# Kernel tuning notes

Hardware: AMD Instinct MI355X
Metric: run time of the kernel (lower is better)

## Reference

```python
import jax, jax.numpy as jnp
import numpy as np

B, S, D, H, FF = 2, 2048, 1024, 16, 4096
HD = D // H
SCALE = 1.0 / np.sqrt(HD).astype(np.float32)
EPS = 1e-5


def _ln(x, g, b):
    m = jnp.mean(x, axis=-1, keepdims=True)
    v = jnp.mean((x - m) ** 2, axis=-1, keepdims=True)
    return (x - m) * jax.lax.rsqrt(v + EPS) * g + b


def setup_inputs() -> dict:
    key = jax.random.key(0)
    ks = jax.random.split(key, 8)
    def lin(k, fan_in, shape):
        return (jax.random.normal(k, shape, jnp.float32) / np.sqrt(fan_in)).astype(jnp.float32)
    return {
        "x": jax.random.normal(ks[0], (B, S, D), jnp.float32),
        "w_qkv": lin(ks[1], D, (D, 3 * D)),          # qkv_proj (no bias)
        "w_o": lin(ks[2], D, (D, D)),                 # out_proj
        "b_o": jnp.zeros((D,), jnp.float32),
        "g1": jnp.ones((D,), jnp.float32),            # attn LayerNorm
        "bt1": jnp.zeros((D,), jnp.float32),
        "w1": lin(ks[3], D, (D, FF)),                 # FFN linear1
        "b1": jnp.zeros((FF,), jnp.float32),
        "w2": lin(ks[4], FF, (FF, D)),                # FFN linear2
        "b2": jnp.zeros((D,), jnp.float32),
        "g2": jnp.ones((D,), jnp.float32),            # FFN LayerNorm
        "bt2": jnp.zeros((D,), jnp.float32),
    }


def reference(x, w_qkv, w_o, b_o, g1, bt1, w1, b1, w2, b2, g2, bt2):
    # --- MultiHeadAttention (post-LN, dropout=eval/identity) ---
    qkv = (x @ w_qkv).reshape(B, S, H, 3 * HD)
    q, k, v = jnp.split(qkv, 3, axis=-1)  # each [B,S,H,HD]
    # kernel_func = scaled softmax over keys
    scores = jnp.einsum("bihd,bjhd->bhij", q, k) * SCALE  # [B,H,S,S]
    attn = jax.nn.softmax(scores, axis=-1)
    ao = jnp.einsum("bhij,bjhd->bihd", attn, v).reshape(B, S, D)
    y = _ln(x + ao @ w_o + b_o, g1, bt1)
    # --- FFN (post-LN) ---
    h = jax.nn.relu(y @ w1 + b1)
    return _ln(y + h @ w2 + b2, g2, bt2)
```

## Files before the change

kernel.cpp:

```cpp
#include <hip/hip_runtime.h>
#include <hip/hip_bf16.h>

#define B_  2
#define S_  2048
#define D_  1024
#define H_  16
#define HD_ 64
#define FF_ 4096
#define NT  (B_ * S_)
#define SCALE_ 0.125f
#define KLOG2E 0.1803368801111f
#define EPS_  1e-5f

typedef __attribute__((ext_vector_type(8))) short bf16x8;
typedef __attribute__((ext_vector_type(4))) float f32x4;

__device__ inline short f2bf(float f) {
    __hip_bfloat16 h = __float2bfloat16(f);
    return __builtin_bit_cast(short, h);
}
__device__ inline float bf2f(unsigned short u) {
    __hip_bfloat16 h = __builtin_bit_cast(__hip_bfloat16, u);
    return __bfloat162float(h);
}

#define GLOBAL_AS __attribute__((address_space(1)))
#define LDS_AS    __attribute__((address_space(3)))

struct DetectArgs { const unsigned short* p[12]; int n[12]; };

__global__ __launch_bounds__(256) void detect_kernel(DetectArgs a, int* flags) {
    const int t = blockIdx.x;
    const unsigned short* s = a.p[t];
    const int cnt = min(a.n[t], 16384);
    const int tid = threadIdx.x;
    int huge = 0, zeven = 0;
    for (int i = tid; i < cnt; i += 256) {
        const unsigned short v = s[i];
        const int e = (v >> 7) & 0xFF;
        if (e >= 142) huge++;
        if (((i & 1) == 0) && ((v & 0x7FFF) == 0)) zeven++;
    }
    __shared__ int sh, sz;
    if (tid == 0) { sh = 0; sz = 0; }
    __syncthreads();
    atomicAdd(&sh, huge);
    atomicAdd(&sz, zeven);
    __syncthreads();
    if (tid == 0) flags[t] = (sh > 0 || sz * 4 > cnt) ? 1 : 0;
}

__global__ __launch_bounds__(256) void conv_bf16_kernel(
    const void* __restrict__ src, unsigned short* __restrict__ dst, int n,
    const int* __restrict__ flags, int fidx)
{
    const int i = blockIdx.x * 256 + threadIdx.x;
    if (i >= n) return;
    if (flags[fidx])
        dst[i] = (unsigned short)f2bf(((const float*)src)[i]);
    else
        dst[i] = ((const unsigned short*)src)[i];
}

__global__ __launch_bounds__(256) void conv_t_kernel(
    const void* __restrict__ src, unsigned short* __restrict__ dst,
    int K, int N, const int* __restrict__ flags, int fidx)
{
    __shared__ short T[32][33];
    const int kt = blockIdx.x * 32, nt = blockIdx.y * 32;
    const int c  = threadIdx.x & 31;
    const int r0 = (threadIdx.x >> 5) * 4;
    const int f  = flags[fidx];
#pragma unroll
    for (int i = 0; i < 4; i++) {
        const int r = r0 + i;
        const size_t gi = (size_t)(kt + r) * N + nt + c;
        short v = f ? f2bf(((const float*)src)[gi])
                    : (short)((const unsigned short*)src)[gi];
        T[c][r] = v;
    }
    __syncthreads();
#pragma unroll
    for (int i = 0; i < 4; i++) {
        const int n = r0 + i;
        dst[(size_t)(nt + n) * K + kt + c] = (unsigned short)T[n][c];
    }
}

struct VecArgs { const void* src[7]; float* dst[7]; int n[7]; int fidx[7]; };

__global__ __launch_bounds__(256) void conv_vecs_kernel(VecArgs a,
                                                        const int* __restrict__ flags) {
#pragma unroll
    for (int v = 0; v < 7; v++) {
        const int f = flags[a.fidx[v]];
        for (int i = blockIdx.x * 256 + threadIdx.x; i < a.n[v]; i += gridDim.x * 256) {
            a.dst[v][i] = f ? ((const float*)a.src[v])[i]
                            : bf2f(((const unsigned short*)a.src[v])[i]);
        }
    }
}

template<bool HAS_BIAS, bool RELU, int RES, bool OUT_F32, bool QSCALE>
__global__ __launch_bounds__(256) void gemm128_kernel(
    const unsigned short* __restrict__ A,
    const unsigned short* __restrict__ Bt,
    const float* __restrict__ bias,
    const unsigned short* __restrict__ resb,
    const float* __restrict__ resf,
    const int* __restrict__ flags,
    void* __restrict__ out,
    int M, int N, int K)
{
    __shared__ short As[128 * 32];
    __shared__ short Bs[128 * 32];

    const int tid  = threadIdx.x;
    const int wave = tid >> 6;
    const int lane = tid & 63;
    const int quad = lane >> 4;
    const int l16  = lane & 15;

    const int row0 = blockIdx.x * 128;
    const int col0 = blockIdx.y * 128;

    const int ldrow = lane >> 2;
    const int ldk   = (lane & 3) * 8;
    const unsigned short* agp0 = A  + (size_t)(row0 + wave * 32 + ldrow) * K + ldk;
    const unsigned short* agp1 = agp0 + (size_t)16 * K;
    const unsigned short* bgp0 = Bt + (size_t)(col0 + wave * 32 + ldrow) * K + ldk;
    const unsigned short* bgp1 = bgp0 + (size_t)16 * K;
    LDS_AS void* alds0 = (LDS_AS void*)&As[wave * 1024 + lane * 8];
    LDS_AS void* alds1 = (LDS_AS void*)&As[wave * 1024 + 512 + lane * 8];
    LDS_AS void* blds0 = (LDS_AS void*)&Bs[wave * 1024 + lane * 8];
    LDS_AS void* blds1 = (LDS_AS void*)&Bs[wave * 1024 + 512 + lane * 8];

    const int wm = (wave >> 1) * 64;
    const int wn = (wave & 1) * 64;

    f32x4 acc[4][4] = {};

    for (int k0 = 0; k0 < K; k0 += 32) {
        __builtin_amdgcn_global_load_lds(
            (const GLOBAL_AS void*)(agp0 + k0), alds0, 16, 0, 0);
        __builtin_amdgcn_global_load_lds(
            (const GLOBAL_AS void*)(agp1 + k0), alds1, 16, 0, 0);
        __builtin_amdgcn_global_load_lds(
            (const GLOBAL_AS void*)(bgp0 + k0), blds0, 16, 0, 0);
        __builtin_amdgcn_global_load_lds(
            (const GLOBAL_AS void*)(bgp1 + k0), blds1, 16, 0, 0);
        __syncthreads();

        bf16x8 af[4], bfr[4];
#pragma unroll
        for (int mi = 0; mi < 4; mi++)
            af[mi] = *reinterpret_cast<const bf16x8*>(
                &As[(wm + mi * 16 + l16) * 32 + quad * 8]);
#pragma unroll
        for (int ni = 0; ni < 4; ni++)
            bfr[ni] = *reinterpret_cast<const bf16x8*>(
                &Bs[(wn + ni * 16 + l16) * 32 + quad * 8]);
#pragma unroll
        for (int mi = 0; mi < 4; mi++)
#pragma unroll
            for (int ni = 0; ni < 4; ni++)
                acc[mi][ni] = __builtin_amdgcn_mfma_f32_16x16x32_bf16(
                    af[mi], bfr[ni], acc[mi][ni], 0, 0, 0);
        __syncthreads();
    }

    int resIsF32 = 0;
    if constexpr (RES == 2) resIsF32 = flags[0];

#pragma unroll
    for (int ni = 0; ni < 4; ni++) {
        const int col = col0 + wn + ni * 16 + l16;
        float badd = 0.f;
        if constexpr (HAS_BIAS) badd = bias[col];
        float qs = 1.f;
        if constexpr (QSCALE)
            qs = (((col0 + wn + ni * 16) % 192) < 64) ? KLOG2E : 1.f;
#pragma unroll
        for (int mi = 0; mi < 4; mi++) {
#pragma unroll
            for (int r = 0; r < 4; r++) {
                const int row = row0 + wm + mi * 16 + quad * 4 + r;
                float v = acc[mi][ni][r] + badd;
                if constexpr (QSCALE) v *= qs;
                if constexpr (RES == 1) {
                    v += bf2f(resb[(size_t)row * N + col]);
                } else if constexpr (RES == 2) {
                    v += resIsF32 ? resf[(size_t)row * N + col]
                                  : bf2f(resb[(size_t)row * N + col]);
                }
                if constexpr (RELU) v = fmaxf(v, 0.f);
                if constexpr (OUT_F32)
                    ((float*)out)[(size_t)row * N + col] = v;
                else
                    ((unsigned short*)out)[(size_t)row * N + col] =
                        (unsigned short)f2bf(v);
            }
        }
    }
}

__global__ __launch_bounds__(256) void gemm128_sk_kernel(
    const unsigned short* __restrict__ A,
    const unsigned short* __restrict__ Bt,
    float* __restrict__ out0,
    float* __restrict__ out1,
    int M, int N, int K)
{
    __shared__ short As[128 * 32];
    __shared__ short Bs[128 * 32];

    const int tid  = threadIdx.x;
    const int wave = tid >> 6;
    const int lane = tid & 63;
    const int quad = lane >> 4;
    const int l16  = lane & 15;

    const int row0 = blockIdx.x * 128;
    const int col0 = blockIdx.y * 128;
    const int z    = blockIdx.z;
    const int Kh   = K >> 1;

    const unsigned short* Az  = A  + (size_t)z * Kh;
    const unsigned short* Btz = Bt + (size_t)z * Kh;
    float* out = z ? out1 : out0;

    const int ldrow = lane >> 2;
    const int ldk   = (lane & 3) * 8;
    const unsigned short* agp0 = Az  + (size_t)(row0 + wave * 32 + ldrow) * K + ldk;
    const unsigned short* agp1 = agp0 + (size_t)16 * K;
    const unsigned short* bgp0 = Btz + (size_t)(col0 + wave * 32 + ldrow) * K + ldk;
    const unsigned short* bgp1 = bgp0 + (size_t)16 * K;
    LDS_AS void* alds0 = (LDS_AS void*)&As[wave * 1024 + lane * 8];
    LDS_AS void* alds1 = (LDS_AS void*)&As[wave * 1024 + 512 + lane * 8];
    LDS_AS void* blds0 = (LDS_AS void*)&Bs[wave * 1024 + lane * 8];
    LDS_AS void* blds1 = (LDS_AS void*)&Bs[wave * 1024 + 512 + lane * 8];

    const int wm = (wave >> 1) * 64;
    const int wn = (wave & 1) * 64;

    f32x4 acc[4][4] = {};

    for (int k0 = 0; k0 < Kh; k0 += 32) {
        __builtin_amdgcn_global_load_lds(
            (const GLOBAL_AS void*)(agp0 + k0), alds0, 16, 0, 0);
        __builtin_amdgcn_global_load_lds(
            (const GLOBAL_AS void*)(agp1 + k0), alds1, 16, 0, 0);
        __builtin_amdgcn_global_load_lds(
            (const GLOBAL_AS void*)(bgp0 + k0), blds0, 16, 0, 0);
        __builtin_amdgcn_global_load_lds(
            (const GLOBAL_AS void*)(bgp1 + k0), blds1, 16, 0, 0);
        __syncthreads();

        bf16x8 af[4], bfr[4];
#pragma unroll
        for (int mi = 0; mi < 4; mi++)
            af[mi] = *reinterpret_cast<const bf16x8*>(
                &As[(wm + mi * 16 + l16) * 32 + quad * 8]);
#pragma unroll
        for (int ni = 0; ni < 4; ni++)
            bfr[ni] = *reinterpret_cast<const bf16x8*>(
                &Bs[(wn + ni * 16 + l16) * 32 + quad * 8]);
#pragma unroll
        for (int mi = 0; mi < 4; mi++)
#pragma unroll
            for (int ni = 0; ni < 4; ni++)
                acc[mi][ni] = __builtin_amdgcn_mfma_f32_16x16x32_bf16(
                    af[mi], bfr[ni], acc[mi][ni], 0, 0, 0);
        __syncthreads();
    }

#pragma unroll
    for (int ni = 0; ni < 4; ni++) {
        const int col = col0 + wn + ni * 16 + l16;
#pragma unroll
        for (int mi = 0; mi < 4; mi++)
#pragma unroll
            for (int r = 0; r < 4; r++) {
                const int row = row0 + wm + mi * 16 + quad * 4 + r;
                out[(size_t)row * N + col] = acc[mi][ni][r];
            }
    }
}

__global__ __launch_bounds__(256) void attn_kernel(
    const unsigned short* __restrict__ qkv,
    unsigned short* __restrict__ ao)
{
    const int qt = blockIdx.x;
    const int h  = blockIdx.y;
    const int b  = blockIdx.z;

    const int tid  = threadIdx.x;
    const int wave = tid >> 6;
    const int lane = tid & 63;
    const int quad = lane >> 4;
    const int l16  = lane & 15;

    __shared__ short Ks[64 * 72];
    __shared__ short Vt[64 * 72];
    __shared__ short Ps[4 * 32 * 72];

    bf16x8 qf[2][2];
#pragma unroll
    for (int mi = 0; mi < 2; mi++) {
        const int qrow = qt * 128 + wave * 32 + mi * 16 + l16;
        const unsigned short* qb = qkv + (size_t)(b * S_ + qrow) * 3072 + h * 192;
        qf[mi][0] = *reinterpret_cast<const bf16x8*>(qb + quad * 8);
        qf[mi][1] = *reinterpret_cast<const bf16x8*>(qb + 32 + quad * 8);
    }

    f32x4 o[2][4] = {};
    float l_[2][4] = {};

    const int skey = tid >> 3;
    const int soct = tid & 7;
    const int vp   = tid >> 3;
    const int kA   = (vp & 15) + ((vp >> 4) << 5);
    const int kB   = kA + 16;
    const int posA = 4 * (vp & 15) + 2 * (vp >> 4);
    const int vwr  = ((posA >> 3) ^ soct) * 8 + (posA & 7);

    const int pb = wave * (32 * 72);

    const unsigned short* kbase0 = qkv + (size_t)(b * S_) * 3072 + h * 192 + 64;
    const unsigned short* vbase0 = qkv + (size_t)(b * S_) * 3072 + h * 192 + 128;

    bf16x8 pk0 = *reinterpret_cast<const bf16x8*>(kbase0 + (size_t)skey * 3072 + soct * 8);
    bf16x8 pk1 = *reinterpret_cast<const bf16x8*>(kbase0 + (size_t)(skey + 32) * 3072 + soct * 8);
    bf16x8 pv0 = *reinterpret_cast<const bf16x8*>(vbase0 + (size_t)kA * 3072 + soct * 8);
    bf16x8 pv1 = *reinterpret_cast<const bf16x8*>(vbase0 + (size_t)kB * 3072 + soct * 8);

    for (int kb = 0; kb < S_; kb += 64) {
        {
            const int woct0 = soct ^ ((skey >> 3) & 1);
            *reinterpret_cast<bf16x8*>(&Ks[skey * 72 + woct0 * 8]) = pk0;
            const int woct1 = soct ^ (((skey + 32) >> 3) & 1);
            *reinterpret_cast<bf16x8*>(&Ks[(skey + 32) * 72 + woct1 * 8]) = pk1;
#pragma unroll
            for (int j = 0; j < 8; j++) {
                const int d = soct * 8 + j;
                const unsigned int val =
                    (unsigned int)(unsigned short)pv0[j] |
                    ((unsigned int)(unsigned short)pv1[j] << 16);
                *reinterpret_cast<unsigned int*>(&Vt[d * 72 + vwr]) = val;
            }
        }
        __syncthreads();

        {
            const int kbn = (kb + 64 < S_) ? kb + 64 : kb;
            pk0 = *reinterpret_cast<const bf16x8*>(
                kbase0 + (size_t)(kbn + skey) * 3072 + soct * 8);
            pk1 = *reinterpret_cast<const bf16x8*>(
                kbase0 + (size_t)(kbn + skey + 32) * 3072 + soct * 8);
            pv0 = *reinterpret_cast<const bf16x8*>(
                vbase0 + (size_t)(kbn + kA) * 3072 + soct * 8);
            pv1 = *reinterpret_cast<const bf16x8*>(
                vbase0 + (size_t)(kbn + kB) * 3072 + soct * 8);
        }

        f32x4 s[2][4] = {};
#pragma unroll
        for (int c2 = 0; c2 < 2; c2++) {
#pragma unroll
            for (int nt = 0; nt < 4; nt++) {
                const int key = nt * 16 + l16;
                const int roct = (c2 * 4 + quad) ^ ((key >> 3) & 1);
                bf16x8 kf = *reinterpret_cast<const bf16x8*>(
                    &Ks[key * 72 + roct * 8]);
                s[0][nt] = __builtin_amdgcn_mfma_f32_16x16x32_bf16(qf[0][c2], kf, s[0][nt], 0, 0, 0);
                s[1][nt] = __builtin_amdgcn_mfma_f32_16x16x32_bf16(qf[1][c2], kf, s[1][nt], 0, 0, 0);
            }
        }

#pragma unroll
        for (int mi = 0; mi < 2; mi++) {
#pragma unroll
            for (int r = 0; r < 4; r++) {
                const int m = mi * 16 + quad * 4 + r;
                float p0 = exp2f(s[mi][0][r]);
                float p1 = exp2f(s[mi][1][r]);
                float p2 = exp2f(s[mi][2][r]);
                float p3 = exp2f(s[mi][3][r]);
                l_[mi][r] += (p0 + p1) + (p2 + p3);
                uint2 w;
                w.x = (unsigned int)(unsigned short)f2bf(p0) |
                      ((unsigned int)(unsigned short)f2bf(p1) << 16);
                w.y = (unsigned int)(unsigned short)f2bf(p2) |
                      ((unsigned int)(unsigned short)f2bf(p3) << 16);
                *reinterpret_cast<uint2*>(&Ps[pb + m * 72 + l16 * 4]) = w;
            }
        }

#pragma unroll
        for (int c2 = 0; c2 < 2; c2++) {
            bf16x8 pf[2];
#pragma unroll
            for (int mi = 0; mi < 2; mi++) {
                const int m = mi * 16 + l16;
                pf[mi] = *reinterpret_cast<const bf16x8*>(
                    &Ps[pb + m * 72 + c2 * 32 + quad * 8]);
            }
#pragma unroll
            for (int ct = 0; ct < 4; ct++) {
                const int row = ct * 16 + l16;
                const int blk = (c2 * 4 + quad) ^ (row >> 3);
                bf16x8 vf = *reinterpret_cast<const bf16x8*>(
                    &Vt[row * 72 + blk * 8]);
                o[0][ct] = __builtin_amdgcn_mfma_f32_16x16x32_bf16(pf[0], vf, o[0][ct], 0, 0, 0);
                o[1][ct] = __builtin_amdgcn_mfma_f32_16x16x32_bf16(pf[1], vf, o[1][ct], 0, 0, 0);
            }
        }
        __syncthreads();
    }

    float rl[2][4];
#pragma unroll
    for (int mi = 0; mi < 2; mi++)
#pragma unroll
        for (int r = 0; r < 4; r++) {
            float l = l_[mi][r];
            l += __shfl_xor(l, 1);
            l += __shfl_xor(l, 2);
            l += __shfl_xor(l, 4);
            l += __shfl_xor(l, 8);
            rl[mi][r] = 1.f / l;
        }

#pragma unroll
    for (int mi = 0; mi < 2; mi++)
#pragma unroll
        for (int ct = 0; ct < 4; ct++)
#pragma unroll
            for (int r = 0; r < 4; r++) {
                const int row = qt * 128 + wave * 32 + mi * 16 + quad * 4 + r;
                ao[(size_t)(b * S_ + row) * D_ + h * HD_ + ct * 16 + l16] =
                    (unsigned short)f2bf(o[mi][ct][r] * rl[mi][r]);
            }
}

template<int RESM, bool FLAG_OUT>
__global__ __launch_bounds__(256) void ln_sum_kernel(
    const float* __restrict__ p0,
    const float* __restrict__ p1,
    const float* __restrict__ bias,
    const unsigned short* __restrict__ resb,
    const float* __restrict__ resf,
    const float* __restrict__ g,
    const float* __restrict__ bt,
    const int* __restrict__ flags,
    void* __restrict__ out)
{
    const int row = blockIdx.x;
    const int tid = threadIdx.x;
    const int c0  = tid * 4;
    const size_t base = (size_t)row * D_ + c0;

    float4 a = *reinterpret_cast<const float4*>(p0 + base);
    float4 bq = *reinterpret_cast<const float4*>(p1 + base);
    float4 bi = *reinterpret_cast<const float4*>(bias + c0);

    float v[4] = {a.x + bq.x + bi.x, a.y + bq.y + bi.y,
                  a.z + bq.z + bi.z, a.w + bq.w + bi.w};

    if constexpr (RESM == 1) {
        if (flags[0]) {
            float4 rv = *reinterpret_cast<const float4*>(resf + base);
            v[0] += rv.x; v[1] += rv.y; v[2] += rv.z; v[3] += rv.w;
        } else {
            uint2 rv = *reinterpret_cast<const uint2*>(resb + base);
            v[0] += bf2f((unsigned short)(rv.x & 0xFFFF));
            v[1] += bf2f((unsigned short)(rv.x >> 16));
            v[2] += bf2f((unsigned short)(rv.y & 0xFFFF));
            v[3] += bf2f((unsigned short)(rv.y >> 16));
        }
    } else {
        uint2 rv = *reinterpret_cast<const uint2*>(resb + base);
        v[0] += bf2f((unsigned short)(rv.x & 0xFFFF));
        v[1] += bf2f((unsigned short)(rv.x >> 16));
        v[2] += bf2f((unsigned short)(rv.y & 0xFFFF));
        v[3] += bf2f((unsigned short)(rv.y >> 16));
    }

    float s = v[0] + v[1] + v[2] + v[3];
    float sq = v[0] * v[0] + v[1] * v[1] + v[2] * v[2] + v[3] * v[3];
#pragma unroll
    for (int msk = 1; msk < 64; msk <<= 1) {
        s += __shfl_xor(s, msk);
        sq += __shfl_xor(sq, msk);
    }
    __shared__ float ss[4], ssq[4];
    if ((tid & 63) == 0) { ss[tid >> 6] = s; ssq[tid >> 6] = sq; }
    __syncthreads();
    s = ss[0] + ss[1] + ss[2] + ss[3];
    sq = ssq[0] + ssq[1] + ssq[2] + ssq[3];

    const float mean = s * (1.f / D_);
    const float var = sq * (1.f / D_) - mean * mean;
    const float rinv = rsqrtf(var + EPS_);

    int outF32 = 0;
    if constexpr (FLAG_OUT) outF32 = flags[0];

#pragma unroll
    for (int i = 0; i < 4; i++) {
        const int c = c0 + i;
        const float val = (v[i] - mean) * rinv * g[c] + bt[c];
        if constexpr (FLAG_OUT) {
            if (outF32) ((float*)out)[(size_t)row * D_ + c] = val;
            else ((unsigned short*)out)[(size_t)row * D_ + c] = (unsigned short)f2bf(val);
        } else {
            ((unsigned short*)out)[(size_t)row * D_ + c] = (unsigned short)f2bf(val);
        }
    }
}

extern "C" void kernel_launch(void* const* d_in, const int* in_sizes, int n_in,
                              void* d_out, int out_size, void* d_ws, size_t ws_size,
                              hipStream_t stream) {
    char* ws = (char*)d_ws;

    int*            flags = (int*)(ws + 0);
    unsigned short* xb    = (unsigned short*)(ws + 256);
    unsigned short* wqkvT = (unsigned short*)(ws + 8388864);
    unsigned short* woT   = (unsigned short*)(ws + 14680320);
    unsigned short* w1T   = (unsigned short*)(ws + 16777472);
    unsigned short* w2T   = (unsigned short*)(ws + 25166080);
    float*          bof   = (float*)(ws + 33554688);
    float*          g1f   = (float*)(ws + 33558784);
    float*          bt1f  = (float*)(ws + 33562880);
    float*          b1f   = (float*)(ws + 33566976);
    float*          b2f   = (float*)(ws + 33583360);
    float*          g2f   = (float*)(ws + 33587456);
    float*          bt2f  = (float*)(ws + 33591552);
    unsigned short* qkv   = (unsigned short*)(ws + 33595648);
    unsigned short* ao    = (unsigned short*)(ws + 256);
    unsigned short* y     = (unsigned short*)(ws + 33595648);
    unsigned short* hbuf  = (unsigned short*)(ws + 41984256);
    float*          part0 = (float*)(ws + 58761472);
    float*          part1 = (float*)(ws + 75538688);
    float*          hpart0= (float*)(ws + 256);

    dim3 blk(256);

    DetectArgs da;
    for (int i = 0; i < 12; i++) {
        da.p[i] = (const unsigned short*)d_in[i];
        da.n[i] = in_sizes[i];
    }
    detect_kernel<<<dim3(12), blk, 0, stream>>>(da, flags);

    conv_bf16_kernel<<<dim3((NT * D_ + 255) / 256), blk, 0, stream>>>(
        d_in[0], xb, NT * D_, flags, 0);
    conv_t_kernel<<<dim3(D_ / 32, 3 * D_ / 32), blk, 0, stream>>>(
        d_in[1], wqkvT, D_, 3 * D_, flags, 1);
    conv_t_kernel<<<dim3(D_ / 32, D_ / 32), blk, 0, stream>>>(
        d_in[2], woT, D_, D_, flags, 2);
    conv_t_kernel<<<dim3(D_ / 32, FF_ / 32), blk, 0, stream>>>(
        d_in[6], w1T, D_, FF_, flags, 6);
    conv_t_kernel<<<dim3(FF_ / 32, D_ / 32), blk, 0, stream>>>(
        d_in[8], w2T, FF_, D_, flags, 8);
    VecArgs va;
    const int vidx[7] = {3, 4, 5, 7, 9, 10, 11};
    float* vdst[7] = {bof, g1f, bt1f, b1f, b2f, g2f, bt2f};
    for (int i = 0; i < 7; i++) {
        va.src[i] = d_in[vidx[i]];
        va.dst[i] = vdst[i];
        va.n[i]   = in_sizes[vidx[i]];
        va.fidx[i] = vidx[i];
    }
    conv_vecs_kernel<<<dim3(16), blk, 0, stream>>>(va, flags);

    gemm128_kernel<false, false, 0, false, true>
        <<<dim3(NT / 128, 3072 / 128), blk, 0, stream>>>(
            xb, wqkvT, nullptr, nullptr, nullptr, flags, qkv, NT, 3072, 1024);

    attn_kernel<<<dim3(S_ / 128, H_, B_), blk, 0, stream>>>(qkv, ao);

    gemm128_sk_kernel<<<dim3(NT / 128, 1024 / 128, 2), blk, 0, stream>>>(
        ao, woT, part0, part1, NT, 1024, 1024);

    ln_sum_kernel<1, false><<<dim3(NT), blk, 0, stream>>>(
        part0, part1, bof, (const unsigned short*)d_in[0], (const float*)d_in[0],
        g1f, bt1f, flags, y);

    gemm128_kernel<true, true, 0, false, false>
        <<<dim3(NT / 128, 4096 / 128), blk, 0, stream>>>(
            y, w1T, b1f, nullptr, nullptr, flags, hbuf, NT, 4096, 1024);

    gemm128_sk_kernel<<<dim3(NT / 128, 1024 / 128, 2), blk, 0, stream>>>(
        hbuf, w2T, hpart0, part1, NT, 1024, 4096);

    ln_sum_kernel<2, true><<<dim3(NT), blk, 0, stream>>>(
        hpart0, part1, b2f, y, nullptr, g2f, bt2f, flags, d_out);
}
```

Baseline: 439.8 us.

## Merge conversion launches, deepen GEMM K-step, compute softmax denominators via MFMA

Several unrelated changes. The conversion launches are merged: the x conversion absorbs the vector conversions, and the four weight transposes become one launch. Both GEMM kernels now load two 32-wide K slices per barrier pair, which halves the number of syncs at the cost of doubled LDS. The attention kernel gets its row sums from an extra MFMA against a vector of ones instead of scalar adds and shuffles, and it packs bf16 pairs with a paired conversion. The LayerNorm store is vectorised.

```diff
diff --git a/kernel.cpp b/kernel.cpp
--- a/kernel.cpp
+++ b/kernel.cpp
@@ -22,6 +22,12 @@
 __device__ inline float bf2f(unsigned short u) {
     __hip_bfloat16 h = __builtin_bit_cast(__hip_bfloat16, u);
     return __bfloat162float(h);
+}
+__device__ inline unsigned int pk2bf(float lo, float hi) {
+    __hip_bfloat162 h = __float22bfloat162_rn(float2{lo, hi});
+    const unsigned short l16 = __builtin_bit_cast(unsigned short, h.x);
+    const unsigned short h16 = __builtin_bit_cast(unsigned short, h.y);
+    return (unsigned int)l16 | ((unsigned int)h16 << 16);
 }
 
 #define GLOBAL_AS __attribute__((address_space(1)))
@@ -50,27 +56,53 @@
     if (tid == 0) flags[t] = (sh > 0 || sz * 4 > cnt) ? 1 : 0;
 }
 
-__global__ __launch_bounds__(256) void conv_bf16_kernel(
+struct VecArgs { const void* src[7]; float* dst[7]; int n[7]; int fidx[7]; };
+
+__global__ __launch_bounds__(256) void conv_x_vecs_kernel(
     const void* __restrict__ src, unsigned short* __restrict__ dst, int n,
-    const int* __restrict__ flags, int fidx)
+    VecArgs a, const int* __restrict__ flags)
 {
     const int i = blockIdx.x * 256 + threadIdx.x;
-    if (i >= n) return;
-    if (flags[fidx])
-        dst[i] = (unsigned short)f2bf(((const float*)src)[i]);
-    else
-        dst[i] = ((const unsigned short*)src)[i];
-}
-
-__global__ __launch_bounds__(256) void conv_t_kernel(
-    const void* __restrict__ src, unsigned short* __restrict__ dst,
-    int K, int N, const int* __restrict__ flags, int fidx)
+    if (i < n) {
+        if (flags[0])
+            dst[i] = (unsigned short)f2bf(((const float*)src)[i]);
+        else
+            dst[i] = ((const unsigned short*)src)[i];
+    }
+    if (blockIdx.x < 7) {
+        const int v = blockIdx.x;
+        const int f = flags[a.fidx[v]];
+        for (int j = threadIdx.x; j < a.n[v]; j += 256) {
+            a.dst[v][j] = f ? ((const float*)a.src[v])[j]
+                            : bf2f(((const unsigned short*)a.src[v])[j]);
+        }
+    }
+}
+
+struct TArgs {
+    const void* src[4]; unsigned short* dst[4];
+    int K[4], N[4], fidx[4], start[5];
+};
+
+__global__ __launch_bounds__(256) void conv_t_all_kernel(
+    TArgs t, const int* __restrict__ flags)
 {
     __shared__ short T[32][33];
-    const int kt = blockIdx.x * 32, nt = blockIdx.y * 32;
+    const int tile = blockIdx.x;
+    int w = 0;
+    if (tile >= t.start[1]) w = 1;
+    if (tile >= t.start[2]) w = 2;
+    if (tile >= t.start[3]) w = 3;
+    const int rel = tile - t.start[w];
+    const int K = t.K[w], N = t.N[w];
+    const int tilesN = N / 32;
+    const int kt = (rel / tilesN) * 32, nt = (rel % tilesN) * 32;
+    const void* src = t.src[w];
+    unsigned short* dst = t.dst[w];
+    const int f = flags[t.fidx[w]];
+
     const int c  = threadIdx.x & 31;
     const int r0 = (threadIdx.x >> 5) * 4;
-    const int f  = flags[fidx];
 #pragma unroll
     for (int i = 0; i < 4; i++) {
         const int r = r0 + i;
@@ -84,20 +116,6 @@
     for (int i = 0; i < 4; i++) {
         const int n = r0 + i;
         dst[(size_t)(nt + n) * K + kt + c] = (unsigned short)T[n][c];
-    }
-}
-
-struct VecArgs { const void* src[7]; float* dst[7]; int n[7]; int fidx[7]; };
-
-__global__ __launch_bounds__(256) void conv_vecs_kernel(VecArgs a,
-                                                        const int* __restrict__ flags) {
-#pragma unroll
-    for (int v = 0; v < 7; v++) {
-        const int f = flags[a.fidx[v]];
-        for (int i = blockIdx.x * 256 + threadIdx.x; i < a.n[v]; i += gridDim.x * 256) {
-            a.dst[v][i] = f ? ((const float*)a.src[v])[i]
-                            : bf2f(((const unsigned short*)a.src[v])[i]);
-        }
     }
 }
 
@@ -112,8 +130,8 @@
     void* __restrict__ out,
     int M, int N, int K)
 {
-    __shared__ short As[128 * 32];
-    __shared__ short Bs[128 * 32];
+    __shared__ short As[2][128 * 32];
+    __shared__ short Bs[2][128 * 32];
 
     const int tid  = threadIdx.x;
     const int wave = tid >> 6;
@@ -130,42 +148,48 @@
     const unsigned short* agp1 = agp0 + (size_t)16 * K;
     const unsigned short* bgp0 = Bt + (size_t)(col0 + wave * 32 + ldrow) * K + ldk;
     const unsigned short* bgp1 = bgp0 + (size_t)16 * K;
-    LDS_AS void* alds0 = (LDS_AS void*)&As[wave * 1024 + lane * 8];
-    LDS_AS void* alds1 = (LDS_AS void*)&As[wave * 1024 + 512 + lane * 8];
-    LDS_AS void* blds0 = (LDS_AS void*)&Bs[wave * 1024 + lane * 8];
-    LDS_AS void* blds1 = (LDS_AS void*)&Bs[wave * 1024 + 512 + lane * 8];
 
     const int wm = (wave >> 1) * 64;
     const int wn = (wave & 1) * 64;
 
     f32x4 acc[4][4] = {};
 
-    for (int k0 = 0; k0 < K; k0 += 32) {
-        __builtin_amdgcn_global_load_lds(
-            (const GLOBAL_AS void*)(agp0 + k0), alds0, 16, 0, 0);
-        __builtin_amdgcn_global_load_lds(
-            (const GLOBAL_AS void*)(agp1 + k0), alds1, 16, 0, 0);
-        __builtin_amdgcn_global_load_lds(
-            (const GLOBAL_AS void*)(bgp0 + k0), blds0, 16, 0, 0);
-        __builtin_amdgcn_global_load_lds(
-            (const GLOBAL_AS void*)(bgp1 + k0), blds1, 16, 0, 0);
+    for (int k0 = 0; k0 < K; k0 += 64) {
+#pragma unroll
+        for (int h = 0; h < 2; h++) {
+            __builtin_amdgcn_global_load_lds(
+                (const GLOBAL_AS void*)(agp0 + k0 + h * 32),
+                (LDS_AS void*)&As[h][wave * 1024 + lane * 8], 16, 0, 0);
+            __builtin_amdgcn_global_load_lds(
+                (const GLOBAL_AS void*)(agp1 + k0 + h * 32),
+                (LDS_AS void*)&As[h][wave * 1024 + 512 + lane * 8], 16, 0, 0);
+            __builtin_amdgcn_global_load_lds(
+                (const GLOBAL_AS void*)(bgp0 + k0 + h * 32),
+                (LDS_AS void*)&Bs[h][wave * 1024 + lane * 8], 16, 0, 0);
+            __builtin_amdgcn_global_load_lds(
+                (const GLOBAL_AS void*)(bgp1 + k0 + h * 32),
+                (LDS_AS void*)&Bs[h][wave * 1024 + 512 + lane * 8], 16, 0, 0);
+        }
         __syncthreads();
 
-        bf16x8 af[4], bfr[4];
-#pragma unroll
-        for (int mi = 0; mi < 4; mi++)
-            af[mi] = *reinterpret_cast<const bf16x8*>(
-                &As[(wm + mi * 16 + l16) * 32 + quad * 8]);
-#pragma unroll
-        for (int ni = 0; ni < 4; ni++)
-            bfr[ni] = *reinterpret_cast<const bf16x8*>(
-                &Bs[(wn + ni * 16 + l16) * 32 + quad * 8]);
-#pragma unroll
-        for (int mi = 0; mi < 4; mi++)
+#pragma unroll
+        for (int h = 0; h < 2; h++) {
+            bf16x8 af[4], bfr[4];
+#pragma unroll
+            for (int mi = 0; mi < 4; mi++)
+                af[mi] = *reinterpret_cast<const bf16x8*>(
+                    &As[h][(wm + mi * 16 + l16) * 32 + quad * 8]);
 #pragma unroll
             for (int ni = 0; ni < 4; ni++)
-                acc[mi][ni] = __builtin_amdgcn_mfma_f32_16x16x32_bf16(
-                    af[mi], bfr[ni], acc[mi][ni], 0, 0, 0);
+                bfr[ni] = *reinterpret_cast<const bf16x8*>(
+                    &Bs[h][(wn + ni * 16 + l16) * 32 + quad * 8]);
+#pragma unroll
+            for (int mi = 0; mi < 4; mi++)
+#pragma unroll
+                for (int ni = 0; ni < 4; ni++)
+                    acc[mi][ni] = __builtin_amdgcn_mfma_f32_16x16x32_bf16(
+                        af[mi], bfr[ni], acc[mi][ni], 0, 0, 0);
+        }
         __syncthreads();
     }
 
@@ -211,8 +235,8 @@
     float* __restrict__ out1,
     int M, int N, int K)
 {
-    __shared__ short As[128 * 32];
-    __shared__ short Bs[128 * 32];
+    __shared__ short As[2][128 * 32];
+    __shared__ short Bs[2][128 * 32];
 
     const int tid  = threadIdx.x;
     const int wave = tid >> 6;
@@ -235,42 +259,48 @@
     const unsigned short* agp1 = agp0 + (size_t)16 * K;
     const unsigned short* bgp0 = Btz + (size_t)(col0 + wave * 32 + ldrow) * K + ldk;
     const unsigned short* bgp1 = bgp0 + (size_t)16 * K;
-    LDS_AS void* alds0 = (LDS_AS void*)&As[wave * 1024 + lane * 8];
-    LDS_AS void* alds1 = (LDS_AS void*)&As[wave * 1024 + 512 + lane * 8];
-    LDS_AS void* blds0 = (LDS_AS void*)&Bs[wave * 1024 + lane * 8];
-    LDS_AS void* blds1 = (LDS_AS void*)&Bs[wave * 1024 + 512 + lane * 8];
 
     const int wm = (wave >> 1) * 64;
     const int wn = (wave & 1) * 64;
 
     f32x4 acc[4][4] = {};
 
-    for (int k0 = 0; k0 < Kh; k0 += 32) {
-        __builtin_amdgcn_global_load_lds(
-            (const GLOBAL_AS void*)(agp0 + k0), alds0, 16, 0, 0);
-        __builtin_amdgcn_global_load_lds(
-            (const GLOBAL_AS void*)(agp1 + k0), alds1, 16, 0, 0);
-        __builtin_amdgcn_global_load_lds(
-            (const GLOBAL_AS void*)(bgp0 + k0), blds0, 16, 0, 0);
-        __builtin_amdgcn_global_load_lds(
-            (const GLOBAL_AS void*)(bgp1 + k0), blds1, 16, 0, 0);
+    for (int k0 = 0; k0 < Kh; k0 += 64) {
+#pragma unroll
+        for (int h = 0; h < 2; h++) {
+            __builtin_amdgcn_global_load_lds(
+                (const GLOBAL_AS void*)(agp0 + k0 + h * 32),
+                (LDS_AS void*)&As[h][wave * 1024 + lane * 8], 16, 0, 0);
+            __builtin_amdgcn_global_load_lds(
+                (const GLOBAL_AS void*)(agp1 + k0 + h * 32),
+                (LDS_AS void*)&As[h][wave * 1024 + 512 + lane * 8], 16, 0, 0);
+            __builtin_amdgcn_global_load_lds(
+                (const GLOBAL_AS void*)(bgp0 + k0 + h * 32),
+                (LDS_AS void*)&Bs[h][wave * 1024 + lane * 8], 16, 0, 0);
+            __builtin_amdgcn_global_load_lds(
+                (const GLOBAL_AS void*)(bgp1 + k0 + h * 32),
+                (LDS_AS void*)&Bs[h][wave * 1024 + 512 + lane * 8], 16, 0, 0);
+        }
         __syncthreads();
 
-        bf16x8 af[4], bfr[4];
-#pragma unroll
-        for (int mi = 0; mi < 4; mi++)
-            af[mi] = *reinterpret_cast<const bf16x8*>(
-                &As[(wm + mi * 16 + l16) * 32 + quad * 8]);
-#pragma unroll
-        for (int ni = 0; ni < 4; ni++)
-            bfr[ni] = *reinterpret_cast<const bf16x8*>(
-                &Bs[(wn + ni * 16 + l16) * 32 + quad * 8]);
-#pragma unroll
-        for (int mi = 0; mi < 4; mi++)
+#pragma unroll
+        for (int h = 0; h < 2; h++) {
+            bf16x8 af[4], bfr[4];
+#pragma unroll
+            for (int mi = 0; mi < 4; mi++)
+                af[mi] = *reinterpret_cast<const bf16x8*>(
+                    &As[h][(wm + mi * 16 + l16) * 32 + quad * 8]);
 #pragma unroll
             for (int ni = 0; ni < 4; ni++)
-                acc[mi][ni] = __builtin_amdgcn_mfma_f32_16x16x32_bf16(
-                    af[mi], bfr[ni], acc[mi][ni], 0, 0, 0);
+                bfr[ni] = *reinterpret_cast<const bf16x8*>(
+                    &Bs[h][(wn + ni * 16 + l16) * 32 + quad * 8]);
+#pragma unroll
+            for (int mi = 0; mi < 4; mi++)
+#pragma unroll
+                for (int ni = 0; ni < 4; ni++)
+                    acc[mi][ni] = __builtin_amdgcn_mfma_f32_16x16x32_bf16(
+                        af[mi], bfr[ni], acc[mi][ni], 0, 0, 0);
+        }
         __syncthreads();
     }
 
@@ -314,8 +344,12 @@
         qf[mi][1] = *reinterpret_cast<const bf16x8*>(qb + 32 + quad * 8);
     }
 
+    bf16x8 vones;
+#pragma unroll
+    for (int j = 0; j < 8; j++) vones[j] = (short)0x3F80;
+
     f32x4 o[2][4] = {};
-    float l_[2][4] = {};
+    f32x4 o_l[2] = {};
 
     const int skey = tid >> 3;
     const int soct = tid & 7;
@@ -383,16 +417,13 @@
 #pragma unroll
             for (int r = 0; r < 4; r++) {
                 const int m = mi * 16 + quad * 4 + r;
-                float p0 = exp2f(s[mi][0][r]);
-                float p1 = exp2f(s[mi][1][r]);
-                float p2 = exp2f(s[mi][2][r]);
-                float p3 = exp2f(s[mi][3][r]);
-                l_[mi][r] += (p0 + p1) + (p2 + p3);
+                const float p0 = exp2f(s[mi][0][r]);
+                const float p1 = exp2f(s[mi][1][r]);
+                const float p2 = exp2f(s[mi][2][r]);
+                const float p3 = exp2f(s[mi][3][r]);
                 uint2 w;
-                w.x = (unsigned int)(unsigned short)f2bf(p0) |
-                      ((unsigned int)(unsigned short)f2bf(p1) << 16);
-                w.y = (unsigned int)(unsigned short)f2bf(p2) |
-                      ((unsigned int)(unsigned short)f2bf(p3) << 16);
+                w.x = pk2bf(p0, p1);
+                w.y = pk2bf(p2, p3);
                 *reinterpret_cast<uint2*>(&Ps[pb + m * 72 + l16 * 4]) = w;
             }
         }
@@ -415,33 +446,26 @@
                 o[0][ct] = __builtin_amdgcn_mfma_f32_16x16x32_bf16(pf[0], vf, o[0][ct], 0, 0, 0);
                 o[1][ct] = __builtin_amdgcn_mfma_f32_16x16x32_bf16(pf[1], vf, o[1][ct], 0, 0, 0);
             }
+            o_l[0] = __builtin_amdgcn_mfma_f32_16x16x32_bf16(pf[0], vones, o_l[0], 0, 0, 0);
+            o_l[1] = __builtin_amdgcn_mfma_f32_16x16x32_bf16(pf[1], vones, o_l[1], 0, 0, 0);
         }
         __syncthreads();
     }
 
-    float rl[2][4];
-#pragma unroll
-    for (int mi = 0; mi < 2; mi++)
-#pragma unroll
-        for (int r = 0; r < 4; r++) {
-            float l = l_[mi][r];
-            l += __shfl_xor(l, 1);
-            l += __shfl_xor(l, 2);
-            l += __shfl_xor(l, 4);
-            l += __shfl_xor(l, 8);
-            rl[mi][r] = 1.f / l;
-        }
-
-#pragma unroll
-    for (int mi = 0; mi < 2; mi++)
+#pragma unroll
+    for (int mi = 0; mi < 2; mi++) {
+        f32x4 rl;
+#pragma unroll
+        for (int r = 0; r < 4; r++) rl[r] = 1.f / o_l[mi][r];
 #pragma unroll
         for (int ct = 0; ct < 4; ct++)
 #pragma unroll
             for (int r = 0; r < 4; r++) {
                 const int row = qt * 128 + wave * 32 + mi * 16 + quad * 4 + r;
                 ao[(size_t)(b * S_ + row) * D_ + h * HD_ + ct * 16 + l16] =
-                    (unsigned short)f2bf(o[mi][ct][r] * rl[mi][r]);
-            }
+                    (unsigned short)f2bf(o[mi][ct][r] * rl[r]);
+            }
+    }
 }
 
 template<int RESM, bool FLAG_OUT>
@@ -504,19 +528,22 @@
     const float var = sq * (1.f / D_) - mean * mean;
     const float rinv = rsqrtf(var + EPS_);
 
+    float w[4];
+#pragma unroll
+    for (int i = 0; i < 4; i++)
+        w[i] = (v[i] - mean) * rinv * g[c0 + i] + bt[c0 + i];
+
     int outF32 = 0;
     if constexpr (FLAG_OUT) outF32 = flags[0];
 
-#pragma unroll
-    for (int i = 0; i < 4; i++) {
-        const int c = c0 + i;
-        const float val = (v[i] - mean) * rinv * g[c] + bt[c];
-        if constexpr (FLAG_OUT) {
-            if (outF32) ((float*)out)[(size_t)row * D_ + c] = val;
-            else ((unsigned short*)out)[(size_t)row * D_ + c] = (unsigned short)f2bf(val);
-        } else {
-            ((unsigned short*)out)[(size_t)row * D_ + c] = (unsigned short)f2bf(val);
-        }
+    if (FLAG_OUT && outF32) {
+        float4 o4 = {w[0], w[1], w[2], w[3]};
+        *reinterpret_cast<float4*>((float*)out + base) = o4;
+    } else {
+        uint2 o2;
+        o2.x = pk2bf(w[0], w[1]);
+        o2.y = pk2bf(w[2], w[3]);
+        *reinterpret_cast<uint2*>((unsigned short*)out + base) = o2;
     }
 }
 
@@ -555,16 +582,6 @@
     }
     detect_kernel<<<dim3(12), blk, 0, stream>>>(da, flags);
 
-    conv_bf16_kernel<<<dim3((NT * D_ + 255) / 256), blk, 0, stream>>>(
-        d_in[0], xb, NT * D_, flags, 0);
-    conv_t_kernel<<<dim3(D_ / 32, 3 * D_ / 32), blk, 0, stream>>>(
-        d_in[1], wqkvT, D_, 3 * D_, flags, 1);
-    conv_t_kernel<<<dim3(D_ / 32, D_ / 32), blk, 0, stream>>>(
-        d_in[2], woT, D_, D_, flags, 2);
-    conv_t_kernel<<<dim3(D_ / 32, FF_ / 32), blk, 0, stream>>>(
-        d_in[6], w1T, D_, FF_, flags, 6);
-    conv_t_kernel<<<dim3(FF_ / 32, D_ / 32), blk, 0, stream>>>(
-        d_in[8], w2T, FF_, D_, flags, 8);
     VecArgs va;
     const int vidx[7] = {3, 4, 5, 7, 9, 10, 11};
     float* vdst[7] = {bof, g1f, bt1f, b1f, b2f, g2f, bt2f};
@@ -574,7 +591,18 @@
         va.n[i]   = in_sizes[vidx[i]];
         va.fidx[i] = vidx[i];
     }
-    conv_vecs_kernel<<<dim3(16), blk, 0, stream>>>(va, flags);
+    conv_x_vecs_kernel<<<dim3((NT * D_ + 255) / 256), blk, 0, stream>>>(
+        d_in[0], xb, NT * D_, va, flags);
+
+    TArgs ta;
+    ta.src[0] = d_in[1]; ta.dst[0] = wqkvT; ta.K[0] = D_;  ta.N[0] = 3 * D_; ta.fidx[0] = 1;
+    ta.src[1] = d_in[2]; ta.dst[1] = woT;   ta.K[1] = D_;  ta.N[1] = D_;     ta.fidx[1] = 2;
+    ta.src[2] = d_in[6]; ta.dst[2] = w1T;   ta.K[2] = D_;  ta.N[2] = FF_;    ta.fidx[2] = 6;
+    ta.src[3] = d_in[8]; ta.dst[3] = w2T;   ta.K[3] = FF_; ta.N[3] = D_;     ta.fidx[3] = 8;
+    ta.start[0] = 0;
+    for (int wI = 0; wI < 4; wI++)
+        ta.start[wI + 1] = ta.start[wI] + (ta.K[wI] / 32) * (ta.N[wI] / 32);
+    conv_t_all_kernel<<<dim3(ta.start[4]), blk, 0, stream>>>(ta, flags);
 
     gemm128_kernel<false, false, 0, false, true>
         <<<dim3(NT / 128, 3072 / 128), blk, 0, stream>>>(
```

After: 392.0 us. -10.9%, faster.
